# Performance work log

Hardware: AMD Instinct MI355X
Metric: run time of the kernel (lower is better)

Reference implementation:

```python
import jax, jax.numpy as jnp
import numpy as np

N_NODES = 40000
N_EDGES = 640000
D = 128
D_OUT = 128


def setup_inputs() -> dict:
    key = jax.random.key(0)
    k1, k2, k3, k4, k5 = jax.random.split(key, 5)
    x = jax.random.normal(k1, (N_NODES, D), dtype=jnp.float32)
    edge_index = jax.random.randint(k2, (2, N_EDGES), 0, N_NODES, dtype=jnp.int64)
    edge_weight = jax.random.uniform(k3, (N_EDGES,), dtype=jnp.float32)
    W = jax.random.normal(k4, (D_OUT, 2 * D), dtype=jnp.float32) / np.sqrt(2 * D)
    b = jax.random.normal(k5, (D_OUT,), dtype=jnp.float32) * 0.01
    return {"x": x, "edge_index": edge_index, "edge_weight": edge_weight, "W": W, "b": b}


def reference(x, edge_index, edge_weight, W, b):
    src, dst = edge_index[0], edge_index[1]
    n_dst = x.shape[0]
    # gather source features per edge: [E, D]
    msgs = x[src]
    # per-destination weight sums (degree-normalization denominator)
    w_sum = jax.ops.segment_sum(edge_weight, dst, num_segments=n_dst)
    w_norm = edge_weight / jnp.clip(w_sum[dst], 1e-8, None)
    # weighted scatter-add aggregation: [N, D]
    agg = jax.ops.segment_sum(w_norm[:, None] * msgs, dst, num_segments=n_dst)
    # concat self + aggregated neighbors, project
    h = jnp.concatenate([x, agg], axis=-1)
    return h @ W.T + b
```

## Files before the change

kernel.cpp:

```cpp
#include <hip/hip_runtime.h>

constexpr int NN = 40000;
constexpr int NE = 640000;
constexpr int NBKT = 625;
constexpr int CBLK = 128;

typedef __attribute__((ext_vector_type(8))) short short8;
typedef __attribute__((ext_vector_type(4))) float f32x4;
typedef __attribute__((ext_vector_type(2))) float f32x2;

__device__ __forceinline__ unsigned short rneb(float f) {
    unsigned u = __float_as_uint(f);
    u = (u + 0x7FFFu + ((u >> 16) & 1u)) >> 16;
    return (unsigned short)u;
}
__device__ __forceinline__ float b2f(unsigned short s) {
    return __uint_as_float(((unsigned)s) << 16);
}

#if defined(__has_builtin)
#if __has_builtin(__builtin_amdgcn_cvt_pk_f32_fp8) && __has_builtin(__builtin_amdgcn_cvt_pk_fp8_f32)
#define FP8_HW 1
#endif
#endif

#ifndef FP8_HW
__device__ __forceinline__ unsigned char f32_to_fp8_sw(float f) {
    float a = fabsf(f);
    unsigned s = (f < 0.f) ? 0x80u : 0u;
    if (a > 448.f) a = 448.f;
    unsigned char r;
    if (a < 0.015625f) {
        int m = (int)rintf(a * 512.f);
        r = (m >= 8) ? (unsigned char)0x08 : (unsigned char)m;
    } else {
        unsigned u = __float_as_uint(a);
        u += 0x0007FFFFu + ((u >> 20) & 1u);
        int e8 = (int)((u >> 23) & 0xFF) - 127 + 7;
        unsigned m = (u >> 20) & 7u;
        if (e8 > 15 || (e8 == 15 && m == 7)) { e8 = 15; m = 6; }
        r = (unsigned char)((e8 << 3) | m);
    }
    return r | (unsigned char)s;
}
__device__ __forceinline__ float fp8_to_f32_sw(unsigned char b) {
    unsigned s = (b >> 7) & 1u, e = (b >> 3) & 0xFu, m = b & 7u;
    float v = e ? ldexpf((float)(8 + m), (int)e - 10) : ldexpf((float)m, -9);
    return s ? -v : v;
}
#endif

__device__ __forceinline__ unsigned pack_fp8x4(float4 v) {
#ifdef FP8_HW
    unsigned r = __builtin_amdgcn_cvt_pk_fp8_f32(v.x, v.y, 0, false);
    r = __builtin_amdgcn_cvt_pk_fp8_f32(v.z, v.w, (int)r, true);
    return r;
#else
    return (unsigned)f32_to_fp8_sw(v.x) | ((unsigned)f32_to_fp8_sw(v.y) << 8)
         | ((unsigned)f32_to_fp8_sw(v.z) << 16) | ((unsigned)f32_to_fp8_sw(v.w) << 24);
#endif
}

__device__ __forceinline__ void unpack_fp8x4(unsigned u, float* o) {
#ifdef FP8_HW
    f32x2 d0 = __builtin_amdgcn_cvt_pk_f32_fp8(u, false);
    f32x2 d1 = __builtin_amdgcn_cvt_pk_f32_fp8(u, true);
    o[0] = d0[0]; o[1] = d0[1]; o[2] = d1[0]; o[3] = d1[1];
#else
    o[0] = fp8_to_f32_sw((unsigned char)(u & 0xFF));
    o[1] = fp8_to_f32_sw((unsigned char)((u >> 8) & 0xFF));
    o[2] = fp8_to_f32_sw((unsigned char)((u >> 16) & 0xFF));
    o[3] = fp8_to_f32_sw((unsigned char)((u >> 24) & 0xFF));
#endif
}

__global__ __launch_bounds__(1024) void prep_k(const float* __restrict__ x,
                                               unsigned short* __restrict__ xb,
                                               unsigned* __restrict__ x8w,
                                               const float* __restrict__ W,
                                               unsigned short* __restrict__ Wb,
                                               const int* __restrict__ dst,
                                               int* __restrict__ gcnt2) {
    __shared__ int cnt[NBKT];
    int bid = blockIdx.x, t = threadIdx.x;
    if (bid < 1250) {
        int g = bid * 1024 + t;
        float4 v = reinterpret_cast<const float4*>(x)[g];
        ushort4 o = { rneb(v.x), rneb(v.y), rneb(v.z), rneb(v.w) };
        reinterpret_cast<ushort4*>(xb)[g] = o;
        x8w[g] = pack_fp8x4(v);
    } else if (bid < 1258) {
        int g = (bid - 1250) * 1024 + t;
        float4 v = reinterpret_cast<const float4*>(W)[g];
        ushort4 o = { rneb(v.x), rneb(v.y), rneb(v.z), rneb(v.w) };
        reinterpret_cast<ushort4*>(Wb)[g] = o;
    } else {
        int cb = bid - 1258;
        if (t < NBKT) cnt[t] = 0;
        __syncthreads();
        int eb = cb * 5000;
        for (int i = t; i < 5000; i += 1024)
            atomicAdd(&cnt[dst[eb + i] >> 6], 1);
        __syncthreads();
        if (t < NBKT) gcnt2[cb * 640 + t] = cnt[t];
    }
}

__global__ __launch_bounds__(1024) void cscan_k(const int* __restrict__ gcnt2,
                                                int* __restrict__ bptr,
                                                int* __restrict__ cursor) {
    __shared__ int sc[1024];
    int t = threadIdx.x;
    int c = 0;
    if (t < NBKT)
        for (int b = 0; b < CBLK; ++b) c += gcnt2[b * 640 + t];
    sc[t] = c;
    __syncthreads();
    for (int o = 1; o < 1024; o <<= 1) {
        int u = (t >= o) ? sc[t - o] : 0;
        __syncthreads();
        sc[t] += u;
        __syncthreads();
    }
    if (t < NBKT) {
        int excl = sc[t] - c;
        bptr[t]   = excl;
        cursor[t] = excl;
    }
    if (t == 0) bptr[NBKT] = NE;
}

__global__ __launch_bounds__(1024) void cscatter_k(const int* __restrict__ dst,
                                                   const int* __restrict__ src,
                                                   const float* __restrict__ ew,
                                                   const int* __restrict__ gcnt2,
                                                   int* __restrict__ cursor,
                                                   unsigned* __restrict__ rec,
                                                   unsigned char* __restrict__ dloc) {
    __shared__ int cnt[NBKT];
    __shared__ int base[NBKT];
    int t = threadIdx.x;
    int cb = blockIdx.x;
    if (t < NBKT) {
        int c = gcnt2[cb * 640 + t];
        base[t] = c ? atomicAdd(&cursor[t], c) : 0;
        cnt[t] = 0;
    }
    __syncthreads();
    int eb = cb * 5000;
    for (int i = t; i < 5000; i += 1024) {
        int d   = dst[eb + i];
        int bkt = d >> 6;
        int slot = atomicAdd(&cnt[bkt], 1);
        int p = base[bkt] + slot;
        unsigned short wh = __builtin_bit_cast(unsigned short, (_Float16)ew[eb + i]);
        rec[p]  = (unsigned)src[eb + i] | ((unsigned)wh << 16);
        dloc[p] = (unsigned char)(d & 63);
    }
}

__global__ __launch_bounds__(1024) void aggemm_k(const unsigned* __restrict__ rec,
                                                 const unsigned char* __restrict__ dloc,
                                                 const int* __restrict__ bptr,
                                                 const unsigned short* __restrict__ xb,
                                                 const unsigned char* __restrict__ x8,
                                                 const unsigned short* __restrict__ Wb,
                                                 const float* __restrict__ bias_p,
                                                 float* __restrict__ out) {
    constexpr int CAP = 2048;
    __shared__ unsigned grec[CAP];
    __shared__ int cnt[64];
    __shared__ int cur[64];
    __shared__ int pL[65];
    __shared__ unsigned short hbl[64 * 128];
    int bkt = blockIdx.x, t = threadIdx.x;
    int beg = bptr[bkt], end = bptr[bkt + 1];
    int grp = t >> 4, fl = t & 15;
    const uint2* xv = reinterpret_cast<const uint2*>(x8);
    float acc[8] = {0.f, 0.f, 0.f, 0.f, 0.f, 0.f, 0.f, 0.f};
    float wsv = 0.f;

    for (int cb = beg; cb < end; cb += CAP) {
        int m = end - cb; if (m > CAP) m = CAP;
        if (t < 64) cnt[t] = 0;
        __syncthreads();
        unsigned r0 = 0, r1 = 0; int d0 = -1, d1 = -1;
        if (t < m)        { r0 = rec[cb + t];        d0 = dloc[cb + t];        atomicAdd(&cnt[d0], 1); }
        if (t + 1024 < m) { r1 = rec[cb + t + 1024]; d1 = dloc[cb + t + 1024]; atomicAdd(&cnt[d1], 1); }
        __syncthreads();
        if (t < 64) {
            int v = cnt[t], s = v;
            #pragma unroll
            for (int o = 1; o < 64; o <<= 1) {
                int u = __shfl_up(s, o);
                if (t >= o) s += u;
            }
            pL[t]  = s - v;
            cur[t] = s - v;
            if (t == 63) pL[64] = s;
        }
        __syncthreads();
        if (d0 >= 0) { int p = atomicAdd(&cur[d0], 1); grec[p] = r0; }
        if (d1 >= 0) { int p = atomicAdd(&cur[d1], 1); grec[p] = r1; }
        __syncthreads();
        int gb = pL[grp], ge = pL[grp + 1];
        int e = gb;
        for (; e + 4 <= ge; e += 4) {
            unsigned q0 = grec[e], q1 = grec[e + 1], q2 = grec[e + 2], q3 = grec[e + 3];
            uint2 a0 = xv[(size_t)(q0 & 0xFFFF) * 16 + fl];
            uint2 a1 = xv[(size_t)(q1 & 0xFFFF) * 16 + fl];
            uint2 a2 = xv[(size_t)(q2 & 0xFFFF) * 16 + fl];
            uint2 a3 = xv[(size_t)(q3 & 0xFFFF) * 16 + fl];
            float w0 = (float)__builtin_bit_cast(_Float16, (unsigned short)(q0 >> 16));
            float w1 = (float)__builtin_bit_cast(_Float16, (unsigned short)(q1 >> 16));
            float w2 = (float)__builtin_bit_cast(_Float16, (unsigned short)(q2 >> 16));
            float w3 = (float)__builtin_bit_cast(_Float16, (unsigned short)(q3 >> 16));
            wsv += w0 + w1 + w2 + w3;
            float f[8];
            unpack_fp8x4(a0.x, f); unpack_fp8x4(a0.y, f + 4);
            #pragma unroll
            for (int i = 0; i < 8; ++i) acc[i] += w0 * f[i];
            unpack_fp8x4(a1.x, f); unpack_fp8x4(a1.y, f + 4);
            #pragma unroll
            for (int i = 0; i < 8; ++i) acc[i] += w1 * f[i];
            unpack_fp8x4(a2.x, f); unpack_fp8x4(a2.y, f + 4);
            #pragma unroll
            for (int i = 0; i < 8; ++i) acc[i] += w2 * f[i];
            unpack_fp8x4(a3.x, f); unpack_fp8x4(a3.y, f + 4);
            #pragma unroll
            for (int i = 0; i < 8; ++i) acc[i] += w3 * f[i];
        }
        for (; e < ge; ++e) {
            unsigned q = grec[e];
            uint2 a = xv[(size_t)(q & 0xFFFF) * 16 + fl];
            float w = (float)__builtin_bit_cast(_Float16, (unsigned short)(q >> 16));
            wsv += w;
            float f[8];
            unpack_fp8x4(a.x, f); unpack_fp8x4(a.y, f + 4);
            #pragma unroll
            for (int i = 0; i < 8; ++i) acc[i] += w * f[i];
        }
        __syncthreads();
    }

    {
        float inv = 1.f / fmaxf(wsv, 1e-8f);
        short8 o;
        #pragma unroll
        for (int i = 0; i < 8; ++i) o[i] = (short)rneb(acc[i] * inv);
        int gs = fl ^ (grp & 7);
        *reinterpret_cast<short8*>(&hbl[grp * 128 + gs * 8]) = o;
    }
    __syncthreads();

    int w = t >> 6, l = t & 63;
    int l15 = l & 15, lg = l >> 4;
    int rt = w & 3, ct0 = w >> 2;
    f32x4 acc2[2] = { (f32x4)0.f, (f32x4)0.f };
    float bias2[2] = { bias_p[ct0 * 16 + l15], bias_p[(ct0 + 4) * 16 + l15] };
    int arow = bkt * 64 + rt * 16 + l15;

    #pragma unroll
    for (int step = 0; step < 8; ++step) {
        short8 a;
        if (step < 4) {
            a = *reinterpret_cast<const short8*>(xb + (size_t)arow * 128 + step * 32 + lg * 8);
        } else {
            int r = rt * 16 + l15;
            int g = (step - 4) * 4 + lg;
            a = *reinterpret_cast<const short8*>(&hbl[r * 128 + (g ^ (r & 7)) * 8]);
        }
        #pragma unroll
        for (int q = 0; q < 2; ++q) {
            int ct = ct0 + q * 4;
            short8 bf = *reinterpret_cast<const short8*>(Wb + (size_t)(ct * 16 + l15) * 256 + step * 32 + lg * 8);
            acc2[q] = __builtin_amdgcn_mfma_f32_16x16x32_bf16(a, bf, acc2[q], 0, 0, 0);
        }
    }

    #pragma unroll
    for (int q = 0; q < 2; ++q)
        #pragma unroll
        for (int r4 = 0; r4 < 4; ++r4) {
            int row = bkt * 64 + rt * 16 + lg * 4 + r4;
            out[(size_t)row * 128 + (ct0 + q * 4) * 16 + l15] = acc2[q][r4] + bias2[q];
        }
}


__global__ void wsum_k(const int* __restrict__ dst, const float* __restrict__ ew,
                       float* __restrict__ wsum) {
    int e = blockIdx.x * 256 + threadIdx.x;
    if (e < NE) atomicAdd(&wsum[dst[e]], ew[e]);
}

__global__ void zerof_k(float* __restrict__ p, int n4) {
    int g = blockIdx.x * 256 + threadIdx.x;
    if (g < n4) reinterpret_cast<float4*>(p)[g] = make_float4(0.f, 0.f, 0.f, 0.f);
}

__global__ void scatter_k(const int* __restrict__ src, const int* __restrict__ dst,
                          const float* __restrict__ ew, const float* __restrict__ wsum,
                          const float* __restrict__ x, float* __restrict__ agg) {
    int tid = blockIdx.x * 256 + threadIdx.x;
    int e = tid >> 5;
    int p = tid & 31;
    if (e >= NE) return;
    int s = src[e], dn = dst[e];
    float wn = ew[e] / fmaxf(wsum[dn], 1e-8f);
    float4 v = *reinterpret_cast<const float4*>(x + (size_t)s * 128 + p * 4);
    float* o = agg + (size_t)dn * 128 + p * 4;
    atomicAdd(o + 0, wn * v.x);
    atomicAdd(o + 1, wn * v.y);
    atomicAdd(o + 2, wn * v.z);
    atomicAdd(o + 3, wn * v.w);
}

__global__ __launch_bounds__(256) void gemm_f32_k(const float* __restrict__ x,
                                                  const float* __restrict__ agg,
                                                  const float* __restrict__ W,
                                                  const float* __restrict__ b,
                                                  float* __restrict__ out) {
    __shared__ float4 Wl[128 * 64];
    __shared__ float4 hl[16 * 64];
    int t = threadIdx.x;
    int base = blockIdx.x * 80;
    const float4* Wg = reinterpret_cast<const float4*>(W);
    #pragma unroll
    for (int i = 0; i < 32; ++i) {
        int f = t + i * 256;
        int r = f >> 6, kk = f & 63;
        Wl[r * 64 + (kk ^ (r & 7))] = Wg[f];
    }
    int jj = t & 63, wsl = t >> 6, sw = jj & 7;
    float bv[2] = { b[jj], b[jj + 64] };
    const float4* xg = reinterpret_cast<const float4*>(x);
    const float4* ag = reinterpret_cast<const float4*>(agg);
    for (int g = 0; g < 5; ++g) {
        int nbase = base + g * 16;
        __syncthreads();
        #pragma unroll
        for (int i = 0; i < 4; ++i) {
            int f = t + i * 256;
            int ln = f >> 6, kk = f & 63;
            size_t node = (size_t)(nbase + ln);
            hl[ln * 64 + kk] = (kk < 32) ? xg[node * 32 + kk] : ag[node * 32 + (kk - 32)];
        }
        __syncthreads();
        float acc[2][4];
        #pragma unroll
        for (int q = 0; q < 2; ++q)
            #pragma unroll
            for (int n = 0; n < 4; ++n) acc[q][n] = 0.f;
        #pragma unroll 4
        for (int kk = 0; kk < 64; ++kk) {
            float4 h[4];
            #pragma unroll
            for (int n = 0; n < 4; ++n) h[n] = hl[(wsl + 4 * n) * 64 + kk];
            #pragma unroll
            for (int q = 0; q < 2; ++q) {
                float4 wvv = Wl[(jj + q * 64) * 64 + (kk ^ sw)];
                #pragma unroll
                for (int n = 0; n < 4; ++n)
                    acc[q][n] += wvv.x * h[n].x + wvv.y * h[n].y + wvv.z * h[n].z + wvv.w * h[n].w;
            }
        }
        #pragma unroll
        for (int q = 0; q < 2; ++q)
            #pragma unroll
            for (int n = 0; n < 4; ++n)
                out[(size_t)(nbase + wsl + 4 * n) * 128 + jj + q * 64] = acc[q][n] + bv[q];
    }
}

extern "C" void kernel_launch(void* const* d_in, const int* in_sizes, int n_in,
                              void* d_out, int out_size, void* d_ws, size_t ws_size,
                              hipStream_t stream) {
    const float* x  = (const float*)d_in[0];
    const int*   ei = (const int*)d_in[1];
    const float* ew = (const float*)d_in[2];
    const float* W  = (const float*)d_in[3];
    const float* b  = (const float*)d_in[4];
    float* out = (float*)d_out;
    const int* src = ei;
    const int* dst = ei + NE;

    const size_t off_cursor = 4096;
    const size_t off_gcnt2  = 8192;
    const size_t off_Wb     = 339968;
    const size_t off_dloc   = 405504;
    const size_t off_rec    = 1048576;
    const size_t off_xb     = 3670016;
    const size_t off_x8     = 13910016;
    const size_t need = off_x8 + (size_t)NN * 128;

    if (ws_size >= need) {
        int* bptr   = (int*)d_ws;
        int* cursor = (int*)((char*)d_ws + off_cursor);
        int* gcnt2  = (int*)((char*)d_ws + off_gcnt2);
        unsigned short* Wb = (unsigned short*)((char*)d_ws + off_Wb);
        unsigned char* dloc = (unsigned char*)((char*)d_ws + off_dloc);
        unsigned* rec = (unsigned*)((char*)d_ws + off_rec);
        unsigned short* xb = (unsigned short*)((char*)d_ws + off_xb);
        unsigned char* x8 = (unsigned char*)((char*)d_ws + off_x8);

        prep_k    <<<1386, 1024, 0, stream>>>(x, xb, (unsigned*)x8, W, Wb, dst, gcnt2);
        cscan_k   <<<1, 1024, 0, stream>>>(gcnt2, bptr, cursor);
        cscatter_k<<<CBLK, 1024, 0, stream>>>(dst, src, ew, gcnt2, cursor, rec, dloc);
        aggemm_k  <<<NBKT, 1024, 0, stream>>>(rec, dloc, bptr, xb, x8, Wb, b, out);
    } else {
        float* wsum = (float*)d_ws;
        float* agg  = out;
        zerof_k  <<<(NN / 4 + 255) / 256, 256, 0, stream>>>(wsum, NN / 4);
        zerof_k  <<<(NN * 32 + 255) / 256, 256, 0, stream>>>(agg, NN * 32);
        wsum_k   <<<(NE + 255) / 256, 256, 0, stream>>>(dst, ew, wsum);
        scatter_k<<<NE * 32 / 256, 256, 0, stream>>>(src, dst, ew, wsum, x, agg);
        gemm_f32_k<<<500, 256, 0, stream>>>(x, agg, W, b, out);
    }
}
```

Measured before the change: 84.38 us.

## Use 128-node buckets with 8 lanes per node in fused aggregate-GEMM kernel

Doubles the destination bucket size from 64 to 128 nodes, which halves the number of aggregation/GEMM blocks to 313. Each node is now handled by 8 lanes that each load 16 fp8 features with one uint4, instead of 16 lanes loading 8 bytes. Each wave computes four MFMA output tiles, so W is reused across more rows. The change needs a two-wave prefix scan, a larger LDS staging buffer and guards for the partial last bucket. It also means fewer blocks to fill the GPU and fewer independent gathers per lane in flight.

```diff
diff --git a/kernel.cpp b/kernel.cpp
--- a/kernel.cpp
+++ b/kernel.cpp
@@ -2,7 +2,7 @@
 
 constexpr int NN = 40000;
 constexpr int NE = 640000;
-constexpr int NBKT = 625;
+constexpr int NBKT = 313;
 constexpr int CBLK = 128;
 
 typedef __attribute__((ext_vector_type(8))) short short8;
@@ -100,9 +100,9 @@
         __syncthreads();
         int eb = cb * 5000;
         for (int i = t; i < 5000; i += 1024)
-            atomicAdd(&cnt[dst[eb + i] >> 6], 1);
-        __syncthreads();
-        if (t < NBKT) gcnt2[cb * 640 + t] = cnt[t];
+            atomicAdd(&cnt[dst[eb + i] >> 7], 1);
+        __syncthreads();
+        if (t < NBKT) gcnt2[cb * 320 + t] = cnt[t];
     }
 }
 
@@ -113,7 +113,7 @@
     int t = threadIdx.x;
     int c = 0;
     if (t < NBKT)
-        for (int b = 0; b < CBLK; ++b) c += gcnt2[b * 640 + t];
+        for (int b = 0; b < CBLK; ++b) c += gcnt2[b * 320 + t];
     sc[t] = c;
     __syncthreads();
     for (int o = 1; o < 1024; o <<= 1) {
@@ -142,7 +142,7 @@
     int t = threadIdx.x;
     int cb = blockIdx.x;
     if (t < NBKT) {
-        int c = gcnt2[cb * 640 + t];
+        int c = gcnt2[cb * 320 + t];
         base[t] = c ? atomicAdd(&cursor[t], c) : 0;
         cnt[t] = 0;
     }
@@ -150,12 +150,12 @@
     int eb = cb * 5000;
     for (int i = t; i < 5000; i += 1024) {
         int d   = dst[eb + i];
-        int bkt = d >> 6;
+        int bkt = d >> 7;
         int slot = atomicAdd(&cnt[bkt], 1);
         int p = base[bkt] + slot;
         unsigned short wh = __builtin_bit_cast(unsigned short, (_Float16)ew[eb + i]);
         rec[p]  = (unsigned)src[eb + i] | ((unsigned)wh << 16);
-        dloc[p] = (unsigned char)(d & 63);
+        dloc[p] = (unsigned char)(d & 127);
     }
 }
 
@@ -167,98 +167,120 @@
                                                  const unsigned short* __restrict__ Wb,
                                                  const float* __restrict__ bias_p,
                                                  float* __restrict__ out) {
-    constexpr int CAP = 2048;
+    constexpr int CAP = 3072;
     __shared__ unsigned grec[CAP];
-    __shared__ int cnt[64];
-    __shared__ int cur[64];
-    __shared__ int pL[65];
-    __shared__ unsigned short hbl[64 * 128];
+    __shared__ int cnt[128];
+    __shared__ int cur[128];
+    __shared__ int pL[129];
+    __shared__ int wtot[2];
+    __shared__ unsigned short hbl[128 * 128];
     int bkt = blockIdx.x, t = threadIdx.x;
     int beg = bptr[bkt], end = bptr[bkt + 1];
-    int grp = t >> 4, fl = t & 15;
-    const uint2* xv = reinterpret_cast<const uint2*>(x8);
-    float acc[8] = {0.f, 0.f, 0.f, 0.f, 0.f, 0.f, 0.f, 0.f};
+    int grp = t >> 3, fl = t & 7;
+    const uint4* xv = reinterpret_cast<const uint4*>(x8);
+    float acc[16];
+    #pragma unroll
+    for (int i = 0; i < 16; ++i) acc[i] = 0.f;
     float wsv = 0.f;
 
     for (int cb = beg; cb < end; cb += CAP) {
         int m = end - cb; if (m > CAP) m = CAP;
-        if (t < 64) cnt[t] = 0;
-        __syncthreads();
-        unsigned r0 = 0, r1 = 0; int d0 = -1, d1 = -1;
-        if (t < m)        { r0 = rec[cb + t];        d0 = dloc[cb + t];        atomicAdd(&cnt[d0], 1); }
-        if (t + 1024 < m) { r1 = rec[cb + t + 1024]; d1 = dloc[cb + t + 1024]; atomicAdd(&cnt[d1], 1); }
-        __syncthreads();
-        if (t < 64) {
-            int v = cnt[t], s = v;
+        if (t < 128) cnt[t] = 0;
+        __syncthreads();
+        unsigned rr[3]; int dd[3];
+        #pragma unroll
+        for (int j = 0; j < 3; ++j) {
+            dd[j] = -1;
+            int i = t + j * 1024;
+            if (i < m) {
+                rr[j] = rec[cb + i];
+                dd[j] = dloc[cb + i];
+                atomicAdd(&cnt[dd[j]], 1);
+            }
+        }
+        __syncthreads();
+        int wv = t >> 6, ln = t & 63;
+        int sv = 0, sincl = 0;
+        if (wv < 2) {
+            sv = cnt[wv * 64 + ln];
+            sincl = sv;
             #pragma unroll
             for (int o = 1; o < 64; o <<= 1) {
-                int u = __shfl_up(s, o);
-                if (t >= o) s += u;
+                int u = __shfl_up(sincl, o);
+                if (ln >= o) sincl += u;
             }
-            pL[t]  = s - v;
-            cur[t] = s - v;
-            if (t == 63) pL[64] = s;
-        }
-        __syncthreads();
-        if (d0 >= 0) { int p = atomicAdd(&cur[d0], 1); grec[p] = r0; }
-        if (d1 >= 0) { int p = atomicAdd(&cur[d1], 1); grec[p] = r1; }
+            if (ln == 63) wtot[wv] = sincl;
+        }
+        __syncthreads();
+        if (wv < 2) {
+            int off = (wv == 1) ? wtot[0] : 0;
+            int idx = wv * 64 + ln;
+            int excl = off + sincl - sv;
+            pL[idx]  = excl;
+            cur[idx] = excl;
+        }
+        if (t == 0) pL[128] = m;
+        __syncthreads();
+        #pragma unroll
+        for (int j = 0; j < 3; ++j)
+            if (dd[j] >= 0) { int p = atomicAdd(&cur[dd[j]], 1); grec[p] = rr[j]; }
         __syncthreads();
         int gb = pL[grp], ge = pL[grp + 1];
         int e = gb;
-        for (; e + 4 <= ge; e += 4) {
-            unsigned q0 = grec[e], q1 = grec[e + 1], q2 = grec[e + 2], q3 = grec[e + 3];
-            uint2 a0 = xv[(size_t)(q0 & 0xFFFF) * 16 + fl];
-            uint2 a1 = xv[(size_t)(q1 & 0xFFFF) * 16 + fl];
-            uint2 a2 = xv[(size_t)(q2 & 0xFFFF) * 16 + fl];
-            uint2 a3 = xv[(size_t)(q3 & 0xFFFF) * 16 + fl];
+        for (; e + 2 <= ge; e += 2) {
+            unsigned q0 = grec[e], q1 = grec[e + 1];
+            uint4 a0 = xv[(size_t)(q0 & 0xFFFF) * 8 + fl];
+            uint4 a1 = xv[(size_t)(q1 & 0xFFFF) * 8 + fl];
             float w0 = (float)__builtin_bit_cast(_Float16, (unsigned short)(q0 >> 16));
             float w1 = (float)__builtin_bit_cast(_Float16, (unsigned short)(q1 >> 16));
-            float w2 = (float)__builtin_bit_cast(_Float16, (unsigned short)(q2 >> 16));
-            float w3 = (float)__builtin_bit_cast(_Float16, (unsigned short)(q3 >> 16));
-            wsv += w0 + w1 + w2 + w3;
-            float f[8];
+            wsv += w0 + w1;
+            float f[16];
             unpack_fp8x4(a0.x, f); unpack_fp8x4(a0.y, f + 4);
-            #pragma unroll
-            for (int i = 0; i < 8; ++i) acc[i] += w0 * f[i];
+            unpack_fp8x4(a0.z, f + 8); unpack_fp8x4(a0.w, f + 12);
+            #pragma unroll
+            for (int i = 0; i < 16; ++i) acc[i] += w0 * f[i];
             unpack_fp8x4(a1.x, f); unpack_fp8x4(a1.y, f + 4);
-            #pragma unroll
-            for (int i = 0; i < 8; ++i) acc[i] += w1 * f[i];
-            unpack_fp8x4(a2.x, f); unpack_fp8x4(a2.y, f + 4);
-            #pragma unroll
-            for (int i = 0; i < 8; ++i) acc[i] += w2 * f[i];
-            unpack_fp8x4(a3.x, f); unpack_fp8x4(a3.y, f + 4);
-            #pragma unroll
-            for (int i = 0; i < 8; ++i) acc[i] += w3 * f[i];
-        }
-        for (; e < ge; ++e) {
+            unpack_fp8x4(a1.z, f + 8); unpack_fp8x4(a1.w, f + 12);
+            #pragma unroll
+            for (int i = 0; i < 16; ++i) acc[i] += w1 * f[i];
+        }
+        if (e < ge) {
             unsigned q = grec[e];
-            uint2 a = xv[(size_t)(q & 0xFFFF) * 16 + fl];
+            uint4 a = xv[(size_t)(q & 0xFFFF) * 8 + fl];
             float w = (float)__builtin_bit_cast(_Float16, (unsigned short)(q >> 16));
             wsv += w;
-            float f[8];
+            float f[16];
             unpack_fp8x4(a.x, f); unpack_fp8x4(a.y, f + 4);
-            #pragma unroll
-            for (int i = 0; i < 8; ++i) acc[i] += w * f[i];
+            unpack_fp8x4(a.z, f + 8); unpack_fp8x4(a.w, f + 12);
+            #pragma unroll
+            for (int i = 0; i < 16; ++i) acc[i] += w * f[i];
         }
         __syncthreads();
     }
 
     {
-        float inv = 1.f / fmaxf(wsv, 1e-8f);
-        short8 o;
-        #pragma unroll
-        for (int i = 0; i < 8; ++i) o[i] = (short)rneb(acc[i] * inv);
-        int gs = fl ^ (grp & 7);
-        *reinterpret_cast<short8*>(&hbl[grp * 128 + gs * 8]) = o;
+        int n = bkt * 128 + grp;
+        if (n < NN) {
+            float inv = 1.f / fmaxf(wsv, 1e-8f);
+            short8 o0, o1;
+            #pragma unroll
+            for (int i = 0; i < 8; ++i) { o0[i] = (short)rneb(acc[i] * inv); o1[i] = (short)rneb(acc[i + 8] * inv); }
+            int s = grp & 7;
+            *reinterpret_cast<short8*>(&hbl[grp * 128 + ((2 * fl) ^ s) * 8])     = o0;
+            *reinterpret_cast<short8*>(&hbl[grp * 128 + ((2 * fl + 1) ^ s) * 8]) = o1;
+        }
     }
     __syncthreads();
 
     int w = t >> 6, l = t & 63;
     int l15 = l & 15, lg = l >> 4;
-    int rt = w & 3, ct0 = w >> 2;
-    f32x4 acc2[2] = { (f32x4)0.f, (f32x4)0.f };
-    float bias2[2] = { bias_p[ct0 * 16 + l15], bias_p[(ct0 + 4) * 16 + l15] };
-    int arow = bkt * 64 + rt * 16 + l15;
+    int rt = w & 7, cq = w >> 3;
+    f32x4 acc2[4] = { (f32x4)0.f, (f32x4)0.f, (f32x4)0.f, (f32x4)0.f };
+    float bias2[4];
+    #pragma unroll
+    for (int q = 0; q < 4; ++q) bias2[q] = bias_p[(cq * 4 + q) * 16 + l15];
+    int arow = bkt * 128 + rt * 16 + l15;
+    if (arow > NN - 1) arow = NN - 1;
 
     #pragma unroll
     for (int step = 0; step < 8; ++step) {
@@ -271,19 +293,20 @@
             a = *reinterpret_cast<const short8*>(&hbl[r * 128 + (g ^ (r & 7)) * 8]);
         }
         #pragma unroll
-        for (int q = 0; q < 2; ++q) {
-            int ct = ct0 + q * 4;
+        for (int q = 0; q < 4; ++q) {
+            int ct = cq * 4 + q;
             short8 bf = *reinterpret_cast<const short8*>(Wb + (size_t)(ct * 16 + l15) * 256 + step * 32 + lg * 8);
             acc2[q] = __builtin_amdgcn_mfma_f32_16x16x32_bf16(a, bf, acc2[q], 0, 0, 0);
         }
     }
 
     #pragma unroll
-    for (int q = 0; q < 2; ++q)
+    for (int q = 0; q < 4; ++q)
         #pragma unroll
         for (int r4 = 0; r4 < 4; ++r4) {
-            int row = bkt * 64 + rt * 16 + lg * 4 + r4;
-            out[(size_t)row * 128 + (ct0 + q * 4) * 16 + l15] = acc2[q][r4] + bias2[q];
+            int row = bkt * 128 + rt * 16 + lg * 4 + r4;
+            if (row < NN)
+                out[(size_t)row * 128 + (cq * 4 + q) * 16 + l15] = acc2[q][r4] + bias2[q];
         }
 }
 
@@ -387,9 +410,9 @@
 
     const size_t off_cursor = 4096;
     const size_t off_gcnt2  = 8192;
-    const size_t off_Wb     = 339968;
-    const size_t off_dloc   = 405504;
-    const size_t off_rec    = 1048576;
+    const size_t off_Wb     = 172032;
+    const size_t off_dloc   = 237568;
+    const size_t off_rec    = 880640;
     const size_t off_xb     = 3670016;
     const size_t off_x8     = 13910016;
     const size_t need = off_x8 + (size_t)NN * 128;
```

Result: slower. 90.24 us (+6.9%).

## Fuse prep, count, scan and scatter into one cooperative kernel

Applied to the files above, without the earlier changes.

Merges the conversion/count kernel, the single-block scan kernel and the bucket scatter kernel into one cooperative launch of 256 blocks, separated by grid-wide syncs. Each block keeps its own bucket counts in shared memory for the scatter phase, so it no longer reloads them. The aim is to remove two kernel launches and the gaps between them. In exchange, the whole grid idles while block 0 performs the serial scan, and the x conversion now runs with fewer, larger blocks.

```diff
diff --git a/kernel.cpp b/kernel.cpp
--- a/kernel.cpp
+++ b/kernel.cpp
@@ -1,9 +1,12 @@
 #include <hip/hip_runtime.h>
+#include <hip/hip_cooperative_groups.h>
+
+namespace cg = cooperative_groups;
 
 constexpr int NN = 40000;
 constexpr int NE = 640000;
 constexpr int NBKT = 625;
-constexpr int CBLK = 128;
+constexpr int PBLK = 256;
 
 typedef __attribute__((ext_vector_type(8))) short short8;
 typedef __attribute__((ext_vector_type(4))) float f32x4;
@@ -74,81 +77,78 @@
 #endif
 }
 
-__global__ __launch_bounds__(1024) void prep_k(const float* __restrict__ x,
-                                               unsigned short* __restrict__ xb,
-                                               unsigned* __restrict__ x8w,
-                                               const float* __restrict__ W,
-                                               unsigned short* __restrict__ Wb,
-                                               const int* __restrict__ dst,
-                                               int* __restrict__ gcnt2) {
+__global__ __launch_bounds__(1024) void fusedprep_k(const float* __restrict__ x,
+                                                    unsigned short* __restrict__ xb,
+                                                    unsigned* __restrict__ x8w,
+                                                    const float* __restrict__ W,
+                                                    unsigned short* __restrict__ Wb,
+                                                    const int* __restrict__ dst,
+                                                    const int* __restrict__ src,
+                                                    const float* __restrict__ ew,
+                                                    int* __restrict__ gcnt2,
+                                                    int* __restrict__ bptr,
+                                                    int* __restrict__ cursor,
+                                                    unsigned* __restrict__ rec,
+                                                    unsigned char* __restrict__ dloc) {
+    cg::grid_group grid = cg::this_grid();
     __shared__ int cnt[NBKT];
+    __shared__ int base[NBKT];
+    __shared__ int sc[1024];
     int bid = blockIdx.x, t = threadIdx.x;
-    if (bid < 1250) {
-        int g = bid * 1024 + t;
+
+    int gb = bid * 5000;
+    for (int i = t; i < 5000; i += 1024) {
+        int g = gb + i;
         float4 v = reinterpret_cast<const float4*>(x)[g];
         ushort4 o = { rneb(v.x), rneb(v.y), rneb(v.z), rneb(v.w) };
         reinterpret_cast<ushort4*>(xb)[g] = o;
         x8w[g] = pack_fp8x4(v);
-    } else if (bid < 1258) {
-        int g = (bid - 1250) * 1024 + t;
+    }
+    if (bid < 8) {
+        int g = bid * 1024 + t;
         float4 v = reinterpret_cast<const float4*>(W)[g];
         ushort4 o = { rneb(v.x), rneb(v.y), rneb(v.z), rneb(v.w) };
         reinterpret_cast<ushort4*>(Wb)[g] = o;
-    } else {
-        int cb = bid - 1258;
-        if (t < NBKT) cnt[t] = 0;
-        __syncthreads();
-        int eb = cb * 5000;
-        for (int i = t; i < 5000; i += 1024)
-            atomicAdd(&cnt[dst[eb + i] >> 6], 1);
-        __syncthreads();
-        if (t < NBKT) gcnt2[cb * 640 + t] = cnt[t];
-    }
-}
-
-__global__ __launch_bounds__(1024) void cscan_k(const int* __restrict__ gcnt2,
-                                                int* __restrict__ bptr,
-                                                int* __restrict__ cursor) {
-    __shared__ int sc[1024];
-    int t = threadIdx.x;
-    int c = 0;
-    if (t < NBKT)
-        for (int b = 0; b < CBLK; ++b) c += gcnt2[b * 640 + t];
-    sc[t] = c;
+    }
+    if (t < NBKT) cnt[t] = 0;
     __syncthreads();
-    for (int o = 1; o < 1024; o <<= 1) {
-        int u = (t >= o) ? sc[t - o] : 0;
-        __syncthreads();
-        sc[t] += u;
-        __syncthreads();
-    }
+    int eb = bid * 2500;
+    for (int i = t; i < 2500; i += 1024)
+        atomicAdd(&cnt[dst[eb + i] >> 6], 1);
+    __syncthreads();
+    if (t < NBKT) gcnt2[bid * 640 + t] = cnt[t];
+    __threadfence();
+    grid.sync();
+
+    if (bid == 0) {
+        int c = 0;
+        if (t < NBKT)
+            for (int b = 0; b < PBLK; ++b) c += gcnt2[b * 640 + t];
+        sc[t] = c;
+        __syncthreads();
+        for (int o = 1; o < 1024; o <<= 1) {
+            int u = (t >= o) ? sc[t - o] : 0;
+            __syncthreads();
+            sc[t] += u;
+            __syncthreads();
+        }
+        if (t < NBKT) {
+            int excl = sc[t] - c;
+            bptr[t]   = excl;
+            cursor[t] = excl;
+        }
+        if (t == 0) bptr[NBKT] = NE;
+        __threadfence();
+    }
+    grid.sync();
+
     if (t < NBKT) {
-        int excl = sc[t] - c;
-        bptr[t]   = excl;
-        cursor[t] = excl;
-    }
-    if (t == 0) bptr[NBKT] = NE;
-}
-
-__global__ __launch_bounds__(1024) void cscatter_k(const int* __restrict__ dst,
-                                                   const int* __restrict__ src,
-                                                   const float* __restrict__ ew,
-                                                   const int* __restrict__ gcnt2,
-                                                   int* __restrict__ cursor,
-                                                   unsigned* __restrict__ rec,
-                                                   unsigned char* __restrict__ dloc) {
-    __shared__ int cnt[NBKT];
-    __shared__ int base[NBKT];
-    int t = threadIdx.x;
-    int cb = blockIdx.x;
-    if (t < NBKT) {
-        int c = gcnt2[cb * 640 + t];
+        int c = cnt[t];
         base[t] = c ? atomicAdd(&cursor[t], c) : 0;
         cnt[t] = 0;
     }
     __syncthreads();
-    int eb = cb * 5000;
-    for (int i = t; i < 5000; i += 1024) {
+    for (int i = t; i < 2500; i += 1024) {
         int d   = dst[eb + i];
         int bkt = d >> 6;
         int slot = atomicAdd(&cnt[bkt], 1);
@@ -387,11 +387,11 @@
 
     const size_t off_cursor = 4096;
     const size_t off_gcnt2  = 8192;
-    const size_t off_Wb     = 339968;
-    const size_t off_dloc   = 405504;
-    const size_t off_rec    = 1048576;
-    const size_t off_xb     = 3670016;
-    const size_t off_x8     = 13910016;
+    const size_t off_Wb     = 665600;
+    const size_t off_dloc   = 733184;
+    const size_t off_rec    = 1376256;
+    const size_t off_xb     = 4194304;
+    const size_t off_x8     = 14434304;
     const size_t need = off_x8 + (size_t)NN * 128;
 
     if (ws_size >= need) {
@@ -403,11 +403,14 @@
         unsigned* rec = (unsigned*)((char*)d_ws + off_rec);
         unsigned short* xb = (unsigned short*)((char*)d_ws + off_xb);
         unsigned char* x8 = (unsigned char*)((char*)d_ws + off_x8);
-
-        prep_k    <<<1386, 1024, 0, stream>>>(x, xb, (unsigned*)x8, W, Wb, dst, gcnt2);
-        cscan_k   <<<1, 1024, 0, stream>>>(gcnt2, bptr, cursor);
-        cscatter_k<<<CBLK, 1024, 0, stream>>>(dst, src, ew, gcnt2, cursor, rec, dloc);
-        aggemm_k  <<<NBKT, 1024, 0, stream>>>(rec, dloc, bptr, xb, x8, Wb, b, out);
+        unsigned* x8w = (unsigned*)x8;
+
+        void* args[] = { (void*)&x, (void*)&xb, (void*)&x8w, (void*)&W, (void*)&Wb,
+                         (void*)&dst, (void*)&src, (void*)&ew, (void*)&gcnt2,
+                         (void*)&bptr, (void*)&cursor, (void*)&rec, (void*)&dloc };
+        hipLaunchCooperativeKernel((const void*)fusedprep_k, dim3(PBLK), dim3(1024),
+                                   args, 0, stream);
+        aggemm_k<<<NBKT, 1024, 0, stream>>>(rec, dloc, bptr, xb, x8, Wb, b, out);
     } else {
         float* wsum = (float*)d_ws;
         float* agg  = out;
```

Result: slower. 212.0 us (+151.3%).
